# Performance work log

Measured on AMD Instinct MI355X. Metric: run time of the kernel, lower is better.

Reference implementation:

```python
import jax, jax.numpy as jnp
import numpy as np

NF1, NF2, HEADS = 64, 64, 8
SCALE = (0.5 * (NF1 + NF2)) ** (-0.5)
EPS = 1e-5


def _ln(x, g, b):
    # LayerNorm over last axis
    mu = jnp.mean(x, axis=-1, keepdims=True)
    var = jnp.mean(jnp.square(x - mu), axis=-1, keepdims=True)
    return (x - mu) * jax.lax.rsqrt(var + EPS) * g + b


def setup_inputs() -> dict:
    key = jax.random.key(0)
    ks = jax.random.split(key, 16)
    B, H, W = 4, 256, 256
    s = 0.05
    return {
        "x1": jax.random.normal(ks[0], (B, NF1, H, W), jnp.float32),
        "x2": jax.random.normal(ks[1], (B, NF2, H, W), jnp.float32),
        "q_w": jax.random.normal(ks[2], (HEADS, NF1), jnp.float32) * s,
        "q_b": jnp.zeros((HEADS,), jnp.float32),
        "k_w": jax.random.normal(ks[3], (HEADS, NF2), jnp.float32) * s,
        "k_b": jnp.zeros((HEADS,), jnp.float32),
        "v_w": jax.random.normal(ks[4], (HEADS, NF1), jnp.float32) * s,
        "v_b": jnp.zeros((HEADS,), jnp.float32),
        "bias": jax.random.normal(ks[5], (1, 1, 1, NF2), jnp.float32),
        "sel_w": jax.random.normal(ks[6], (HEADS, NF2), jnp.float32) * s,
        "sel_b": jnp.zeros((HEADS,), jnp.float32),
        "fan_w": jax.random.normal(ks[7], (NF1, HEADS), jnp.float32) * s,
        "fan_b": jnp.zeros((NF1,), jnp.float32),
        "gamma": jax.random.normal(ks[8], (1, NF1, 1, 1), jnp.float32),
        "ln1_w": jnp.ones((NF1,), jnp.float32),
        "ln1_b": jnp.zeros((NF1,), jnp.float32),
        "ln2_w": jnp.ones((NF2,), jnp.float32),
        "ln2_b": jnp.zeros((NF2,), jnp.float32),
    }


def reference(x1, x2, q_w, q_b, k_w, k_b, v_w, v_b, bias, sel_w, sel_b,
              fan_w, fan_b, gamma, ln1_w, ln1_b, ln2_w, ln2_b):
    # Work in NHWC internally (matches the permute(0,2,3,1) pattern).
    x1n = _ln(jnp.transpose(x1, (0, 2, 3, 1)), ln1_w, ln1_b)  # [B,H,W,nf1]
    x2n = _ln(jnp.transpose(x2, (0, 2, 3, 1)), ln2_w, ln2_b)  # [B,H,W,nf2]

    # 1x1 convs == per-pixel linear projections
    q = jnp.einsum('bhwc,dc->bhwd', x1n, q_w) + q_b  # [B,H,W,heads]
    k = jnp.einsum('bhwc,dc->bhwd', x2n, k_w) + k_b  # [B,H,W,heads]
    v = jnp.einsum('bhwc,dc->bhwd', x1n, v_w) + v_b  # [B,H,W,heads]

    # row-wise attention over W: scores [B,H,W,W]
    attn = jax.nn.softmax(SCALE * jnp.einsum('bhwd,bhud->bhwu', q, k), axis=-1)
    mp = jnp.einsum('bhwu,bhud->bhwd', attn, v)  # [B,H,W,heads]

    # bias selector: Linear(nf2 -> heads) applied to learned bias [1,1,1,nf2]
    mp = mp + (jnp.einsum('ijkc,dc->ijkd', bias, sel_w) + sel_b)

    fo = jnp.einsum('bhwd,od->bhwo', mp, fan_w) + fan_b  # [B,H,W,nf1]
    g = jnp.transpose(gamma, (0, 2, 3, 1))  # [1,1,1,nf1]
    out = x1n + g * fo
    return jnp.transpose(out, (0, 3, 1, 2))  # NCHW [B,nf1,H,W]
```

## Files before the change

kernel.cpp:

```cpp
#include <hip/hip_runtime.h>

#define BDIM 512
#define HH 256
#define WW 256
#define NF 64
#define NH 8
#define HW (HH * WW)

typedef __attribute__((ext_vector_type(8))) short short8v;
typedef __attribute__((ext_vector_type(4))) float f32x4;

__device__ __forceinline__ unsigned short f2bf(float f) {
  const unsigned u = __float_as_uint(f);
  return (unsigned short)((u + 0x7fffu + ((u >> 16) & 1u)) >> 16);
}

__device__ __forceinline__ uint2 exp2_pack(f32x4 sv) {
  const float e0 = __builtin_amdgcn_exp2f(sv.x);
  const float e1 = __builtin_amdgcn_exp2f(sv.y);
  const float e2 = __builtin_amdgcn_exp2f(sv.z);
  const float e3 = __builtin_amdgcn_exp2f(sv.w);
  uint2 r;
  r.x = (unsigned)f2bf(e0) | ((unsigned)f2bf(e1) << 16);
  r.y = (unsigned)f2bf(e2) | ((unsigned)f2bf(e3) << 16);
  return r;
}

struct __align__(16) Smem {
  unsigned short kb16[WW * 8];
  unsigned short qb16[WW * 8];
  unsigned short vb16[8][264];
  unsigned short pstage[8][640];
  float mpst[WW][10];
  float murst[WW][2];
  float Sq1[NH], Sq0[NH], Sk1[NH], Sk0[NH], Sv1[NH], Sv0[NH], bsel[NH];
};

__global__ __launch_bounds__(BDIM, 8)
void cc_attn_kernel(const float* __restrict__ x1,
                    const float* __restrict__ x2,
                    const float* __restrict__ q_w,
                    const float* __restrict__ q_b,
                    const float* __restrict__ k_w,
                    const float* __restrict__ k_b,
                    const float* __restrict__ v_w,
                    const float* __restrict__ v_b,
                    const float* __restrict__ bias,
                    const float* __restrict__ sel_w,
                    const float* __restrict__ sel_b,
                    const float* __restrict__ fan_w,
                    const float* __restrict__ fan_b,
                    const float* __restrict__ gma,
                    const float* __restrict__ ln1w,
                    const float* __restrict__ ln1b,
                    const float* __restrict__ ln2w,
                    const float* __restrict__ ln2b,
                    float* __restrict__ out)
{
  __shared__ Smem s;
  const int tid  = threadIdx.x;
  const int role = tid >> 8;
  const int pix  = tid & 255;
  const int b = blockIdx.x >> 8;
  const int h = blockIdx.x & 255;
  const size_t rowbase = ((size_t)(b * NF) * HH + h) * WW;
  const size_t base = rowbase + pix;

  if (tid < NH) {
    const int d = tid;
    float s1q = 0, s0q = 0, s1k = 0, s0k = 0, s1v = 0, s0v = 0, bs = 0;
    for (int c = 0; c < NF; c++) {
      const float qw = q_w[d * NF + c], kw = k_w[d * NF + c], vw = v_w[d * NF + c];
      s1q += ln1w[c] * qw; s0q += ln1b[c] * qw;
      s1k += ln2w[c] * kw; s0k += ln2b[c] * kw;
      s1v += ln1w[c] * vw; s0v += ln1b[c] * vw;
      bs  += bias[c] * sel_w[d * NF + c];
    }
    s.Sq1[d] = s1q; s.Sq0[d] = s0q + q_b[d];
    s.Sk1[d] = s1k; s.Sk0[d] = s0k + k_b[d];
    s.Sv1[d] = s1v; s.Sv0[d] = s0v + v_b[d];
    s.bsel[d] = bs + sel_b[d];
  }

  float sum = 0.f, ss = 0.f;
  float ta[NH] = {}, tb[NH] = {};
  if (role == 0) {
    const float* p = x2 + base;
    #pragma unroll 4
    for (int c = 0; c < NF; c++) {
      const float xv = p[(size_t)c * HW];
      const float yv = xv * ln2w[c];
      sum += xv; ss += xv * xv;
      #pragma unroll
      for (int d = 0; d < NH; d++) ta[d] += yv * k_w[d * NF + c];
    }
  } else {
    const float* p = x1 + base;
    #pragma unroll 4
    for (int c = 0; c < NF; c++) {
      const float xv = p[(size_t)c * HW];
      const float yv = xv * ln1w[c];
      sum += xv; ss += xv * xv;
      #pragma unroll
      for (int d = 0; d < NH; d++) {
        ta[d] += yv * q_w[d * NF + c];
        tb[d] += yv * v_w[d * NF + c];
      }
    }
  }
  const float mu   = sum * (1.f / NF);
  const float rstd = rsqrtf(ss * (1.f / NF) - mu * mu + 1e-5f);
  if (role == 1) { s.murst[pix][0] = mu; s.murst[pix][1] = rstd; }

  __syncthreads();

  const float QS = 0.125f * 1.44269504088896340736f;
  if (role == 0) {
    unsigned short pk[8];
    #pragma unroll
    for (int d = 0; d < NH; d++)
      pk[d] = f2bf(rstd * (ta[d] - mu * s.Sk1[d]) + s.Sk0[d]);
    *reinterpret_cast<short8v*>(&s.kb16[pix * 8]) = *reinterpret_cast<short8v*>(pk);
  } else {
    unsigned short pk[8];
    #pragma unroll
    for (int d = 0; d < NH; d++) {
      pk[d] = f2bf((rstd * (ta[d] - mu * s.Sq1[d]) + s.Sq0[d]) * QS);
      s.vb16[d][pix] = f2bf(rstd * (tb[d] - mu * s.Sv1[d]) + s.Sv0[d]);
    }
    *reinterpret_cast<short8v*>(&s.qb16[pix * 8]) = *reinterpret_cast<short8v*>(pk);
  }

  __syncthreads();

  {
    const int lane = tid & 63;
    const int wid  = tid >> 6;
    const int g    = lane >> 4;
    const int r16  = lane & 15;
    const int qb0  = wid * 32;

    const short8v zero8 = {0,0,0,0,0,0,0,0};
    const short8v ones8 = {(short)0x3F80,(short)0x3F80,(short)0x3F80,(short)0x3F80,
                           (short)0x3F80,(short)0x3F80,(short)0x3F80,(short)0x3F80};
    const f32x4 zero4 = {0.f, 0.f, 0.f, 0.f};

    short8v bq0 = zero8, bq1 = zero8;
    if (g == 0) {
      bq0 = *reinterpret_cast<const short8v*>(&s.qb16[(qb0 + r16) * 8]);
      bq1 = *reinterpret_cast<const short8v*>(&s.qb16[(qb0 + 16 + r16) * 8]);
    }

    f32x4 o0 = zero4, o1 = zero4;
    unsigned short* __restrict__ pst = &s.pstage[wid][0];
    const int wr_off = r16 * 40 + g * 4;
    const int rd_off = r16 * 40 + g * 8;

    #pragma unroll 2
    for (int ch = 0; ch < 8; ++ch) {
      const int u0 = ch * 32;
      short8v ak0 = zero8, ak1 = zero8;
      if (g == 0) {
        ak0 = *reinterpret_cast<const short8v*>(&s.kb16[(u0 + r16) * 8]);
        ak1 = *reinterpret_cast<const short8v*>(&s.kb16[(u0 + 16 + r16) * 8]);
      }
      short8v av = zero8;
      if (r16 < 8)       av = *reinterpret_cast<const short8v*>(&s.vb16[r16][u0 + g * 8]);
      else if (r16 == 8) av = ones8;

      {
        f32x4 s0 = __builtin_amdgcn_mfma_f32_16x16x32_bf16(ak0, bq0, zero4, 0, 0, 0);
        f32x4 s1 = __builtin_amdgcn_mfma_f32_16x16x32_bf16(ak1, bq0, zero4, 0, 0, 0);
        const uint2 p0 = exp2_pack(s0);
        const uint2 p1 = exp2_pack(s1);
        *reinterpret_cast<uint2*>(&pst[wr_off])      = p0;
        *reinterpret_cast<uint2*>(&pst[wr_off + 16]) = p1;
        const short8v bp = *reinterpret_cast<const short8v*>(&pst[rd_off]);
        o0 = __builtin_amdgcn_mfma_f32_16x16x32_bf16(av, bp, o0, 0, 0, 0);
      }
      {
        f32x4 s0 = __builtin_amdgcn_mfma_f32_16x16x32_bf16(ak0, bq1, zero4, 0, 0, 0);
        f32x4 s1 = __builtin_amdgcn_mfma_f32_16x16x32_bf16(ak1, bq1, zero4, 0, 0, 0);
        const uint2 p0 = exp2_pack(s0);
        const uint2 p1 = exp2_pack(s1);
        *reinterpret_cast<uint2*>(&pst[wr_off])      = p0;
        *reinterpret_cast<uint2*>(&pst[wr_off + 16]) = p1;
        const short8v bp = *reinterpret_cast<const short8v*>(&pst[rd_off]);
        o1 = __builtin_amdgcn_mfma_f32_16x16x32_bf16(av, bp, o1, 0, 0, 0);
      }
    }

    {
      const int q0 = qb0 + r16;
      const int q1 = qb0 + 16 + r16;
      if (g == 0) {
        *reinterpret_cast<float2*>(&s.mpst[q0][0]) = make_float2(o0.x, o0.y);
        *reinterpret_cast<float2*>(&s.mpst[q0][2]) = make_float2(o0.z, o0.w);
        *reinterpret_cast<float2*>(&s.mpst[q1][0]) = make_float2(o1.x, o1.y);
        *reinterpret_cast<float2*>(&s.mpst[q1][2]) = make_float2(o1.z, o1.w);
      } else if (g == 1) {
        *reinterpret_cast<float2*>(&s.mpst[q0][4]) = make_float2(o0.x, o0.y);
        *reinterpret_cast<float2*>(&s.mpst[q0][6]) = make_float2(o0.z, o0.w);
        *reinterpret_cast<float2*>(&s.mpst[q1][4]) = make_float2(o1.x, o1.y);
        *reinterpret_cast<float2*>(&s.mpst[q1][6]) = make_float2(o1.z, o1.w);
      } else if (g == 2) {
        s.mpst[q0][8] = o0.x;
        s.mpst[q1][8] = o1.x;
      }
    }
  }

  __syncthreads();

  {
    const int qg = pix;
    const float rl = 1.0f / s.mpst[qg][8];
    float mp[NH];
    #pragma unroll
    for (int d = 0; d < NH; d++) mp[d] = s.mpst[qg][d] * rl + s.bsel[d];

    const float m1 = s.murst[qg][0];
    const float r1 = s.murst[qg][1];
    const int c0 = role * 32;
    const float* p = x1 + base;
    #pragma unroll 4
    for (int cc = 0; cc < 32; cc++) {
      const int c = c0 + cc;
      float fo = fan_b[c];
      #pragma unroll
      for (int d = 0; d < NH; d++) fo += mp[d] * fan_w[c * NH + d];
      const float xv  = p[(size_t)c * HW];
      const float x1n = (xv - m1) * r1 * ln1w[c] + ln1b[c];
      out[base + (size_t)c * HW] = x1n + gma[c] * fo;
    }
  }
}

extern "C" void kernel_launch(void* const* d_in, const int* in_sizes, int n_in,
                              void* d_out, int out_size, void* d_ws, size_t ws_size,
                              hipStream_t stream) {
  (void)in_sizes; (void)n_in; (void)d_ws; (void)ws_size; (void)out_size;
  const float* x1    = (const float*)d_in[0];
  const float* x2    = (const float*)d_in[1];
  const float* q_w   = (const float*)d_in[2];
  const float* q_b   = (const float*)d_in[3];
  const float* k_w   = (const float*)d_in[4];
  const float* k_b   = (const float*)d_in[5];
  const float* v_w   = (const float*)d_in[6];
  const float* v_b   = (const float*)d_in[7];
  const float* bias  = (const float*)d_in[8];
  const float* sel_w = (const float*)d_in[9];
  const float* sel_b = (const float*)d_in[10];
  const float* fan_w = (const float*)d_in[11];
  const float* fan_b = (const float*)d_in[12];
  const float* gma   = (const float*)d_in[13];
  const float* ln1w  = (const float*)d_in[14];
  const float* ln1b  = (const float*)d_in[15];
  const float* ln2w  = (const float*)d_in[16];
  const float* ln2b  = (const float*)d_in[17];

  hipLaunchKernelGGL(cc_attn_kernel, dim3(4 * HH), dim3(BDIM), 0, stream,
                     x1, x2, q_w, q_b, k_w, k_b, v_w, v_b, bias, sel_w, sel_b,
                     fan_w, fan_b, gma, ln1w, ln1b, ln2w, ln2b,
                     (float*)d_out);
}
```

Before: 75.52 us.

## Compute Q/K/V projections with bf16 MFMA instead of scalar FMA loops

Replaces the per-thread scalar 64x8 (and 64x16) projection loops with MFMA 16x16x32 bf16 matrix multiplies. Each wave loads x1 and x2 for 32 pixels, computes LayerNorm statistics via cross-lane shuffles, and stages bf16 weights in shared memory. Shared memory is unioned to reuse weight and stat buffers, so LDS use stays about the same. The aim is to cut the VALU work of the projection phase. In exchange, the inputs are now rounded to bf16 before projection, which adds precision error, and there is an extra barrier plus a scatter of results.

```diff
diff --git a/kernel.cpp b/kernel.cpp
--- a/kernel.cpp
+++ b/kernel.cpp
@@ -6,6 +6,7 @@
 #define NF 64
 #define NH 8
 #define HW (HH * WW)
+#define WBP 68
 
 typedef __attribute__((ext_vector_type(8))) short short8v;
 typedef __attribute__((ext_vector_type(4))) float f32x4;
@@ -30,8 +31,14 @@
   unsigned short kb16[WW * 8];
   unsigned short qb16[WW * 8];
   unsigned short vb16[8][264];
-  unsigned short pstage[8][640];
-  float mpst[WW][10];
+  union {
+    struct { unsigned short wb1[16 * WBP]; unsigned short wb2[16 * WBP]; } w;
+    float mpst[WW][10];
+  } u1;
+  union {
+    unsigned short pstage[8][640];
+    float murst2[WW][2];
+  } u2;
   float murst[WW][2];
   float Sq1[NH], Sq0[NH], Sk1[NH], Sk0[NH], Sv1[NH], Sv0[NH], bsel[NH];
 };
@@ -59,12 +66,17 @@
 {
   __shared__ Smem s;
   const int tid  = threadIdx.x;
-  const int role = tid >> 8;
-  const int pix  = tid & 255;
+  const int lane = tid & 63;
+  const int wid  = tid >> 6;
+  const int g    = lane >> 4;
+  const int r16  = lane & 15;
   const int b = blockIdx.x >> 8;
   const int h = blockIdx.x & 255;
   const size_t rowbase = ((size_t)(b * NF) * HH + h) * WW;
-  const size_t base = rowbase + pix;
+
+  const float QS = 0.125f * 1.44269504088896340736f;
+  const short8v zero8 = {0,0,0,0,0,0,0,0};
+  const f32x4 zero4 = {0.f, 0.f, 0.f, 0.f};
 
   if (tid < NH) {
     const int d = tid;
@@ -82,68 +94,100 @@
     s.bsel[d] = bs + sel_b[d];
   }
 
-  float sum = 0.f, ss = 0.f;
-  float ta[NH] = {}, tb[NH] = {};
-  if (role == 0) {
-    const float* p = x2 + base;
-    #pragma unroll 4
-    for (int c = 0; c < NF; c++) {
-      const float xv = p[(size_t)c * HW];
-      const float yv = xv * ln2w[c];
-      sum += xv; ss += xv * xv;
+  for (int i = tid; i < 16 * NF; i += BDIM) {
+    const int n = i >> 6, c = i & 63;
+    const float w1 = (n < 8 ? q_w[n * NF + c] : v_w[(n - 8) * NF + c]) * ln1w[c];
+    const float w2 = (n < 8 ? k_w[n * NF + c] * ln2w[c] : 0.f);
+    s.u1.w.wb1[n * WBP + c] = f2bf(w1);
+    s.u1.w.wb2[n * WBP + c] = f2bf(w2);
+  }
+
+  __syncthreads();
+
+  f32x4 accQV0 = zero4, accQV1 = zero4, accK0 = zero4, accK1 = zero4;
+  float s1[2] = {0.f, 0.f}, q1[2] = {0.f, 0.f};
+  float s2[2] = {0.f, 0.f}, q2p[2] = {0.f, 0.f};
+
+  #pragma unroll 1
+  for (int kc = 0; kc < 2; ++kc) {
+    const short8v bqv = *reinterpret_cast<const short8v*>(&s.u1.w.wb1[r16 * WBP + kc * 32 + g * 8]);
+    const short8v bk  = *reinterpret_cast<const short8v*>(&s.u1.w.wb2[r16 * WBP + kc * 32 + g * 8]);
+    #pragma unroll
+    for (int m = 0; m < 2; ++m) {
+      const int gp = wid * 32 + m * 16 + r16;
+      const float* p1 = x1 + rowbase + gp + (size_t)(kc * 32 + g * 8) * HW;
+      const float* p2 = x2 + rowbase + gp + (size_t)(kc * 32 + g * 8) * HW;
+      float xv[8], yv[8];
       #pragma unroll
-      for (int d = 0; d < NH; d++) ta[d] += yv * k_w[d * NF + c];
-    }
-  } else {
-    const float* p = x1 + base;
-    #pragma unroll 4
-    for (int c = 0; c < NF; c++) {
-      const float xv = p[(size_t)c * HW];
-      const float yv = xv * ln1w[c];
-      sum += xv; ss += xv * xv;
+      for (int i = 0; i < 8; ++i) xv[i] = p1[(size_t)i * HW];
       #pragma unroll
-      for (int d = 0; d < NH; d++) {
-        ta[d] += yv * q_w[d * NF + c];
-        tb[d] += yv * v_w[d * NF + c];
-      }
-    }
-  }
-  const float mu   = sum * (1.f / NF);
-  const float rstd = rsqrtf(ss * (1.f / NF) - mu * mu + 1e-5f);
-  if (role == 1) { s.murst[pix][0] = mu; s.murst[pix][1] = rstd; }
+      for (int i = 0; i < 8; ++i) yv[i] = p2[(size_t)i * HW];
+      unsigned short pk1[8], pk2[8];
+      float la = 0.f, lb = 0.f, lc = 0.f, ld = 0.f;
+      #pragma unroll
+      for (int i = 0; i < 8; ++i) {
+        la += xv[i]; lb += xv[i] * xv[i]; pk1[i] = f2bf(xv[i]);
+        lc += yv[i]; ld += yv[i] * yv[i]; pk2[i] = f2bf(yv[i]);
+      }
+      s1[m] += la; q1[m] += lb; s2[m] += lc; q2p[m] += ld;
+      const short8v a1 = *reinterpret_cast<const short8v*>(pk1);
+      const short8v a2 = *reinterpret_cast<const short8v*>(pk2);
+      if (m == 0) {
+        accQV0 = __builtin_amdgcn_mfma_f32_16x16x32_bf16(a1, bqv, accQV0, 0, 0, 0);
+        accK0  = __builtin_amdgcn_mfma_f32_16x16x32_bf16(a2, bk,  accK0,  0, 0, 0);
+      } else {
+        accQV1 = __builtin_amdgcn_mfma_f32_16x16x32_bf16(a1, bqv, accQV1, 0, 0, 0);
+        accK1  = __builtin_amdgcn_mfma_f32_16x16x32_bf16(a2, bk,  accK1,  0, 0, 0);
+      }
+    }
+  }
+
+  #pragma unroll
+  for (int m = 0; m < 2; ++m) {
+    float a = s1[m] + __shfl_xor(s1[m], 16);   a += __shfl_xor(a, 32);
+    float v = q1[m] + __shfl_xor(q1[m], 16);   v += __shfl_xor(v, 32);
+    float c = s2[m] + __shfl_xor(s2[m], 16);   c += __shfl_xor(c, 32);
+    float d = q2p[m] + __shfl_xor(q2p[m], 16); d += __shfl_xor(d, 32);
+    if (g == 0) {
+      const int gp = wid * 32 + m * 16 + r16;
+      const float mu1v = a * (1.f / NF);
+      s.murst[gp][0] = mu1v;
+      s.murst[gp][1] = rsqrtf(v * (1.f / NF) - mu1v * mu1v + 1e-5f);
+      const float mu2v = c * (1.f / NF);
+      s.u2.murst2[gp][0] = mu2v;
+      s.u2.murst2[gp][1] = rsqrtf(d * (1.f / NF) - mu2v * mu2v + 1e-5f);
+    }
+  }
 
   __syncthreads();
 
-  const float QS = 0.125f * 1.44269504088896340736f;
-  if (role == 0) {
-    unsigned short pk[8];
+  #pragma unroll
+  for (int m = 0; m < 2; ++m) {
+    const f32x4 aQV = m ? accQV1 : accQV0;
+    const f32x4 aK  = m ? accK1  : accK0;
     #pragma unroll
-    for (int d = 0; d < NH; d++)
-      pk[d] = f2bf(rstd * (ta[d] - mu * s.Sk1[d]) + s.Sk0[d]);
-    *reinterpret_cast<short8v*>(&s.kb16[pix * 8]) = *reinterpret_cast<short8v*>(pk);
-  } else {
-    unsigned short pk[8];
-    #pragma unroll
-    for (int d = 0; d < NH; d++) {
-      pk[d] = f2bf((rstd * (ta[d] - mu * s.Sq1[d]) + s.Sq0[d]) * QS);
-      s.vb16[d][pix] = f2bf(rstd * (tb[d] - mu * s.Sv1[d]) + s.Sv0[d]);
-    }
-    *reinterpret_cast<short8v*>(&s.qb16[pix * 8]) = *reinterpret_cast<short8v*>(pk);
+    for (int j = 0; j < 4; ++j) {
+      const int pix = wid * 32 + m * 16 + g * 4 + j;
+      const float mu1v = s.murst[pix][0], rs1v = s.murst[pix][1];
+      if (r16 < 8) {
+        const float mu2v = s.u2.murst2[pix][0], rs2v = s.u2.murst2[pix][1];
+        const float qv = (rs1v * (aQV[j] - mu1v * s.Sq1[r16]) + s.Sq0[r16]) * QS;
+        s.qb16[pix * 8 + r16] = f2bf(qv);
+        const float kv = rs2v * (aK[j] - mu2v * s.Sk1[r16]) + s.Sk0[r16];
+        s.kb16[pix * 8 + r16] = f2bf(kv);
+      } else {
+        const float vv = rs1v * (aQV[j] - mu1v * s.Sv1[r16 - 8]) + s.Sv0[r16 - 8];
+        s.vb16[r16 - 8][pix] = f2bf(vv);
+      }
+    }
   }
 
   __syncthreads();
 
   {
-    const int lane = tid & 63;
-    const int wid  = tid >> 6;
-    const int g    = lane >> 4;
-    const int r16  = lane & 15;
-    const int qb0  = wid * 32;
-
-    const short8v zero8 = {0,0,0,0,0,0,0,0};
+    const int qb0 = wid * 32;
     const short8v ones8 = {(short)0x3F80,(short)0x3F80,(short)0x3F80,(short)0x3F80,
                            (short)0x3F80,(short)0x3F80,(short)0x3F80,(short)0x3F80};
-    const f32x4 zero4 = {0.f, 0.f, 0.f, 0.f};
 
     short8v bq0 = zero8, bq1 = zero8;
     if (g == 0) {
@@ -152,7 +196,7 @@
     }
 
     f32x4 o0 = zero4, o1 = zero4;
-    unsigned short* __restrict__ pst = &s.pstage[wid][0];
+    unsigned short* __restrict__ pst = &s.u2.pstage[wid][0];
     const int wr_off = r16 * 40 + g * 4;
     const int rd_off = r16 * 40 + g * 8;
 
@@ -170,9 +214,9 @@
 
       {
         f32x4 s0 = __builtin_amdgcn_mfma_f32_16x16x32_bf16(ak0, bq0, zero4, 0, 0, 0);
-        f32x4 s1 = __builtin_amdgcn_mfma_f32_16x16x32_bf16(ak1, bq0, zero4, 0, 0, 0);
+        f32x4 s1v = __builtin_amdgcn_mfma_f32_16x16x32_bf16(ak1, bq0, zero4, 0, 0, 0);
         const uint2 p0 = exp2_pack(s0);
-        const uint2 p1 = exp2_pack(s1);
+        const uint2 p1 = exp2_pack(s1v);
         *reinterpret_cast<uint2*>(&pst[wr_off])      = p0;
         *reinterpret_cast<uint2*>(&pst[wr_off + 16]) = p1;
         const short8v bp = *reinterpret_cast<const short8v*>(&pst[rd_off]);
@@ -180,9 +224,9 @@
       }
       {
         f32x4 s0 = __builtin_amdgcn_mfma_f32_16x16x32_bf16(ak0, bq1, zero4, 0, 0, 0);
-        f32x4 s1 = __builtin_amdgcn_mfma_f32_16x16x32_bf16(ak1, bq1, zero4, 0, 0, 0);
+        f32x4 s1v = __builtin_amdgcn_mfma_f32_16x16x32_bf16(ak1, bq1, zero4, 0, 0, 0);
         const uint2 p0 = exp2_pack(s0);
-        const uint2 p1 = exp2_pack(s1);
+        const uint2 p1 = exp2_pack(s1v);
         *reinterpret_cast<uint2*>(&pst[wr_off])      = p0;
         *reinterpret_cast<uint2*>(&pst[wr_off + 16]) = p1;
         const short8v bp = *reinterpret_cast<const short8v*>(&pst[rd_off]);
@@ -192,20 +236,20 @@
 
     {
       const int q0 = qb0 + r16;
-      const int q1 = qb0 + 16 + r16;
+      const int q1i = qb0 + 16 + r16;
       if (g == 0) {
-        *reinterpret_cast<float2*>(&s.mpst[q0][0]) = make_float2(o0.x, o0.y);
-        *reinterpret_cast<float2*>(&s.mpst[q0][2]) = make_float2(o0.z, o0.w);
-        *reinterpret_cast<float2*>(&s.mpst[q1][0]) = make_float2(o1.x, o1.y);
-        *reinterpret_cast<float2*>(&s.mpst[q1][2]) = make_float2(o1.z, o1.w);
+        *reinterpret_cast<float2*>(&s.u1.mpst[q0][0]) = make_float2(o0.x, o0.y);
+        *reinterpret_cast<float2*>(&s.u1.mpst[q0][2]) = make_float2(o0.z, o0.w);
+        *reinterpret_cast<float2*>(&s.u1.mpst[q1i][0]) = make_float2(o1.x, o1.y);
+        *reinterpret_cast<float2*>(&s.u1.mpst[q1i][2]) = make_float2(o1.z, o1.w);
       } else if (g == 1) {
-        *reinterpret_cast<float2*>(&s.mpst[q0][4]) = make_float2(o0.x, o0.y);
-        *reinterpret_cast<float2*>(&s.mpst[q0][6]) = make_float2(o0.z, o0.w);
-        *reinterpret_cast<float2*>(&s.mpst[q1][4]) = make_float2(o1.x, o1.y);
-        *reinterpret_cast<float2*>(&s.mpst[q1][6]) = make_float2(o1.z, o1.w);
+        *reinterpret_cast<float2*>(&s.u1.mpst[q0][4]) = make_float2(o0.x, o0.y);
+        *reinterpret_cast<float2*>(&s.u1.mpst[q0][6]) = make_float2(o0.z, o0.w);
+        *reinterpret_cast<float2*>(&s.u1.mpst[q1i][4]) = make_float2(o1.x, o1.y);
+        *reinterpret_cast<float2*>(&s.u1.mpst[q1i][6]) = make_float2(o1.z, o1.w);
       } else if (g == 2) {
-        s.mpst[q0][8] = o0.x;
-        s.mpst[q1][8] = o1.x;
+        s.u1.mpst[q0][8] = o0.x;
+        s.u1.mpst[q1i][8] = o1.x;
       }
     }
   }
@@ -213,16 +257,18 @@
   __syncthreads();
 
   {
-    const int qg = pix;
-    const float rl = 1.0f / s.mpst[qg][8];
+    const int qg = tid & 255;
+    const int role = tid >> 8;
+    const float rl = 1.0f / s.u1.mpst[qg][8];
     float mp[NH];
     #pragma unroll
-    for (int d = 0; d < NH; d++) mp[d] = s.mpst[qg][d] * rl + s.bsel[d];
+    for (int d = 0; d < NH; d++) mp[d] = s.u1.mpst[qg][d] * rl + s.bsel[d];
 
     const float m1 = s.murst[qg][0];
     const float r1 = s.murst[qg][1];
     const int c0 = role * 32;
-    const float* p = x1 + base;
+    const size_t qbase = rowbase + qg;
+    const float* p = x1 + qbase;
     #pragma unroll 4
     for (int cc = 0; cc < 32; cc++) {
       const int c = c0 + cc;
@@ -231,7 +277,7 @@
       for (int d = 0; d < NH; d++) fo += mp[d] * fan_w[c * NH + d];
       const float xv  = p[(size_t)c * HW];
       const float x1n = (xv - m1) * r1 * ln1w[c] + ln1b[c];
-      out[base + (size_t)c * HW] = x1n + gma[c] * fo;
+      out[qbase + (size_t)c * HW] = x1n + gma[c] * fo;
     }
   }
 }
```

Result: slower. 126.3 us (+67.3%).
